# Kernel optimization log

Hardware: AMD Instinct MI355X
Metric: run time of the kernel (lower is better)

The kernel has to match this reference:

```python
import jax, jax.numpy as jnp
import numpy as np

SPLINE_ORDER = 3
BN_EPS = 1e-5


def make_grid(grid_size, lo=-1.0, hi=1.0):
    # torch KANLinear grid: uniform on [lo,hi] extended by spline_order knots each side
    h = (hi - lo) / grid_size
    return jnp.arange(-SPLINE_ORDER, grid_size + SPLINE_ORDER + 1, dtype=jnp.float32) * h + lo


def b_splines(x, grid, k=SPLINE_ORDER):
    # x: [...], grid: [G+2k+1] -> bases [..., G+k] (Cox-de Boor recursion)
    x = x[..., None]
    bases = ((x >= grid[:-1]) & (x < grid[1:])).astype(x.dtype)
    for j in range(1, k + 1):
        left = (x - grid[: -(j + 1)]) / (grid[j:-1] - grid[: -(j + 1)])
        right = (grid[j + 1:] - x) / (grid[j + 1:] - grid[1:-j])
        bases = left * bases[..., :-1] + right * bases[..., 1:]
    return bases


def extract_patches(x, d):
    # 3x3 dilated sliding windows, stride 1, padding == dilation -> same HxW
    B, C, H, W = x.shape
    xp = jnp.pad(x, ((0, 0), (0, 0), (d, d), (d, d)))
    pats = [xp[:, :, ki * d:ki * d + H, kj * d:kj * d + W]
            for ki in range(3) for kj in range(3)]
    return jnp.stack(pats, axis=-1)  # [B,C,H,W,9] (kh-major, matching torch Unfold)


def batchnorm(x, g, b):
    # training-mode BN (torch default forward): batch statistics, biased variance
    mean = x.mean(axis=(0, 2, 3), keepdims=True)
    var = x.var(axis=(0, 2, 3), keepdims=True)
    return (x - mean) / jnp.sqrt(var + BN_EPS) * g[None, :, None, None] + b[None, :, None, None]


def se_block(x, w1, w2):
    y = x.mean(axis=(2, 3))                                  # [B,C]
    y = jax.nn.sigmoid(jax.nn.relu(y @ w1.T) @ w2.T)         # [B,C]
    return x * y[:, :, None, None]


def kan_conv(x, base_w, spline_w, grid, dilation):
    # one KANLinear(9->1) per (out,in) channel pair, summed over in channels
    p = extract_patches(x, dilation)                          # [B,Ci,H,W,9]
    base = jnp.einsum('bihwk,oik->bohw', jax.nn.silu(p), base_w)
    bs = b_splines(p, grid)                                   # [B,Ci,H,W,9,G+k]
    spl = jnp.einsum('bihwkg,oikg->bohw', bs, spline_w)
    return base + spl


def kan_branch(x, base_w, spline_w, grid, dilation, bn_g, bn_b, se_w1, se_w2):
    y = kan_conv(x, base_w, spline_w, grid, dilation)
    y = jax.nn.relu(batchnorm(y, bn_g, bn_b))
    return se_block(y, se_w1, se_w2)


def setup_inputs() -> dict:
    key = jax.random.key(0)
    ks = jax.random.split(key, 16)
    B, Ci, Co, H, W = 2, 64, 64, 64, 64
    r = Co // 16
    d = {"x": jax.random.normal(ks[0], (B, Ci, H, W), jnp.float32)}
    for i, (bname, G) in enumerate([(6, 3), (12, 6), (18, 9)]):
        kk = jax.random.split(ks[1 + i], 4)
        d[f"base_w{bname}"] = jax.random.normal(kk[0], (Co, Ci, 9), jnp.float32) / np.sqrt(9.0 * Ci)
        d[f"spline_w{bname}"] = jax.random.normal(kk[1], (Co, Ci, 9, G + SPLINE_ORDER), jnp.float32) * (0.1 / np.sqrt(9.0 * Ci))
        d[f"bn{bname}_g"] = jnp.ones((Co,), jnp.float32)
        d[f"bn{bname}_b"] = jnp.zeros((Co,), jnp.float32)
        d[f"se{bname}_w1"] = jax.random.normal(kk[2], (r, Co), jnp.float32) / np.sqrt(Co)
        d[f"se{bname}_w2"] = jax.random.normal(kk[3], (Co, r), jnp.float32) / np.sqrt(r)
    d["gp_conv_w"] = jax.random.normal(ks[4], (Co, Ci), jnp.float32) / np.sqrt(Ci)
    d["gp_conv_b"] = jnp.zeros((Co,), jnp.float32)
    d["gp_bn_g"] = jnp.ones((Co,), jnp.float32)
    d["gp_bn_b"] = jnp.zeros((Co,), jnp.float32)
    d["gp_se_w1"] = jax.random.normal(ks[5], (r, Co), jnp.float32) / np.sqrt(Co)
    d["gp_se_w2"] = jax.random.normal(ks[6], (Co, r), jnp.float32) / np.sqrt(r)
    d["fuse_w"] = jax.random.normal(ks[7], (Co, 4 * Co), jnp.float32) / np.sqrt(4.0 * Co)
    d["fuse_b"] = jnp.zeros((Co,), jnp.float32)
    d["fuse_bn_g"] = jnp.ones((Co,), jnp.float32)
    d["fuse_bn_b"] = jnp.zeros((Co,), jnp.float32)
    return d


def reference(x, base_w6, spline_w6, bn6_g, bn6_b, se6_w1, se6_w2,
              base_w12, spline_w12, bn12_g, bn12_b, se12_w1, se12_w2,
              base_w18, spline_w18, bn18_g, bn18_b, se18_w1, se18_w2,
              gp_conv_w, gp_conv_b, gp_bn_g, gp_bn_b, gp_se_w1, gp_se_w2,
              fuse_w, fuse_b, fuse_bn_g, fuse_bn_b):
    B, Ci, H, W = x.shape
    # global-pool branch: avgpool -> 1x1 conv -> BN -> ReLU -> SE -> bilinear
    # upsample (1x1 source => pure broadcast, align_corners irrelevant)
    gp = x.mean(axis=(2, 3)) @ gp_conv_w.T + gp_conv_b      # [B,Co]
    gp = gp[:, :, None, None]
    gp = jax.nn.relu(batchnorm(gp, gp_bn_g, gp_bn_b))
    gp = se_block(gp, gp_se_w1, gp_se_w2)
    gp = jnp.broadcast_to(gp, (B, gp.shape[1], H, W))
    # KAN dilated branches
    b6 = kan_branch(x, base_w6, spline_w6, make_grid(3), 6, bn6_g, bn6_b, se6_w1, se6_w2)
    b12 = kan_branch(x, base_w12, spline_w12, make_grid(6), 12, bn12_g, bn12_b, se12_w1, se12_w2)
    b18 = kan_branch(x, base_w18, spline_w18, make_grid(9), 18, bn18_g, bn18_b, se18_w1, se18_w2)
    cat = jnp.concatenate([b6, b12, b18, gp], axis=1)        # [B,4Co,H,W]
    out = jnp.einsum('bihw,oi->bohw', cat, fuse_w) + fuse_b[None, :, None, None]
    out = jax.nn.relu(batchnorm(out, fuse_bn_g, fuse_bn_b))
    return out
```

## Files before the change

### kernel.cpp

```cpp
#include <hip/hip_runtime.h>
#include <hip/hip_bf16.h>
#include <math.h>

#define DEV __device__ __forceinline__

static constexpr int HW  = 4096;
static constexpr int POS = 8192;
static constexpr int SLAB = 6 * 64 * 4096;

typedef __attribute__((ext_vector_type(8)))  short short8;
typedef __attribute__((ext_vector_type(16))) float floatx16;
typedef __attribute__((ext_vector_type(4)))  unsigned int uint4v;

template<int G>
DEV void bsplines(float x, float* out ) {
  const float h = 2.0f / (float)G;
  float knot[G + 7];
#pragma unroll
  for (int t = 0; t < G + 7; ++t) knot[t] = -1.0f + (float)(t - 3) * h;
  float bb[G + 6];
#pragma unroll
  for (int t = 0; t < G + 6; ++t) bb[t] = (x >= knot[t] && x < knot[t + 1]) ? 1.0f : 0.0f;
#pragma unroll
  for (int j = 1; j <= 3; ++j) {
    const float inv = (float)G / (2.0f * (float)j);
#pragma unroll
    for (int t = 0; t < G + 6 - j; ++t) {
      float left  = (x - knot[t]) * inv;
      float right = (knot[t + j + 1] - x) * inv;
      bb[t] = left * bb[t] + right * bb[t + 1];
    }
  }
#pragma unroll
  for (int t = 0; t < G + 3; ++t) out[t] = bb[t];
}

DEV float sigmoidf_(float x) { return 1.0f / (1.0f + __expf(-x)); }

DEV float block_reduce_256(float v, float* sb) {
  __syncthreads();
#pragma unroll
  for (int off = 32; off > 0; off >>= 1) v += __shfl_down(v, off, 64);
  int lane = threadIdx.x & 63, wid = threadIdx.x >> 6;
  if (lane == 0) sb[wid] = v;
  __syncthreads();
  return sb[0] + sb[1] + sb[2] + sb[3];
}


template<int CF>
DEV void wprep_body(const float* __restrict__ base_w, const float* __restrict__ spline_w,
                    __hip_bfloat16* __restrict__ Wt, int bid) {
  constexpr int KC = 64 * CF;
  int lin = bid * 256 + threadIdx.x;
  int ic = lin % KC;
  int rest = lin / KC;
  int o = rest & 63, tap = rest >> 6;
  int c = ic % CF, i = ic / CF;
  float v = (c == 0) ? base_w[(o * 64 + i) * 9 + tap]
                     : spline_w[((o * 64 + i) * 9 + tap) * (CF - 1) + (c - 1)];
  int s = ic >> 4, kk = ic & 15, q = kk >> 3, r = kk & 7, hh = o >> 5;
  int l = q * 32 + (o & 31);
  Wt[(size_t)tap * (64 * KC) + s * 1024 + hh * 512 + l * 8 + r] = __float2bfloat16(v);
}

template<int G>
DEV void c0r_body(int ki, const float* __restrict__ sw, float* __restrict__ out,
                  float* shmem ) {
  constexpr int NB = G + 3;
  int o = threadIdx.x & 63, part = threadIdx.x >> 6;
  float b0[NB];
  bsplines<G>(0.0f, b0);
  float s = 0.0f;
  for (int kj = 0; kj < 3; ++kj) {
    int tap = ki * 3 + kj;
    for (int i = part * 16; i < part * 16 + 16; ++i) {
      const float* p = sw + ((size_t)(o * 64 + i) * 9 + tap) * NB;
#pragma unroll
      for (int c = 0; c < NB; ++c) s += p[c] * b0[c];
    }
  }
  shmem[part * 64 + o] = s;
  __syncthreads();
  if (part == 0)
    out[ki * 64 + o] = shmem[o] + shmem[64 + o] + shmem[128 + o] + shmem[192 + o];
}

template<int G, int RB>
DEV void feat_stage(float xv, float s, __hip_bfloat16* lds, int ws, int i) {
  constexpr int CF = G + 4;
  constexpr int RS = 64 * CF + 16;
  float bas[G + 3];
  bsplines<G>(xv, bas);
  __hip_bfloat16* d = lds + RB + ws * RS + i * CF;
  d[0] = __float2bfloat16(s);
#pragma unroll
  for (int c = 1; c < CF; ++c) d[c] = __float2bfloat16(bas[c - 1]);
}

template<int CF, int D, int RBu>
DEV void feat_copy(__hip_bfloat16* __restrict__ F, int b, int h, int wg, const uint4v* l) {
  constexpr int WP = 64 + 2 * D;
  constexpr int KC = 64 * CF;
  uint4v* g = (uint4v*)(F + (size_t)(b * 64 + h) * WP * KC);
  for (int t = threadIdx.x; t < 32 * CF; t += 256) {
    int sc = t >> 3, r = t & 7, wl = r >> 1, k4 = r & 1;
    g[(size_t)(sc * WP + D + wg * 4 + wl) * 2 + k4] = l[RBu + wl * (8 * CF + 2) + sc * 2 + k4];
  }
}

DEV void feat_interior(const float* __restrict__ x, __hip_bfloat16* F0, __hip_bfloat16* F1,
                       __hip_bfloat16* F2, int bid, __hip_bfloat16* lds) {
  int tid = threadIdx.x;
  int ws = tid & 3, i = tid >> 2;
  int wg = bid & 15, h = (bid >> 4) & 63, b = bid >> 10;
  int w = wg * 4 + ws;
  float xv = x[((size_t)(b * 64 + i) * 64 + h) * 64 + w];
  float s = xv * sigmoidf_(xv);
  feat_stage<3, 0>(xv, s, lds, ws, i);
  feat_stage<6, 1856>(xv, s, lds, ws, i);
  feat_stage<9, 4480>(xv, s, lds, ws, i);
  __syncthreads();
  const uint4v* l = (const uint4v*)lds;
  feat_copy<7, 6, 0>(F0, b, h, wg, l);
  feat_copy<10, 12, 232>(F1, b, h, wg, l);
  feat_copy<13, 18, 560>(F2, b, h, wg, l);
}

template<int G, int D>
DEV void halo_body(__hip_bfloat16* __restrict__ F, int bidl, __hip_bfloat16* ldsb) {
  constexpr int CF = G + 4;
  constexpr int WP = 64 + 2 * D;
  constexpr int KC = 64 * CF;
  constexpr int PW = 8 * CF;
  constexpr int D2 = 2 * D;
  int tid = threadIdx.x;
  float bas0[G + 3];
  bsplines<G>(0.0f, bas0);
  for (int k = tid; k < KC; k += 256) {
    int c = k % CF;
    float v = 0.0f;
#pragma unroll
    for (int cc = 1; cc < CF; ++cc) v = (c == cc) ? bas0[cc - 1] : v;
    ldsb[k] = __float2bfloat16(v);
  }
  __syncthreads();
  const uint4v* l = (const uint4v*)ldsb;
  uint4v* g = (uint4v*)F;
#pragma unroll
  for (int u = 0; u < 16; ++u) {
    int t = bidl * 4096 + u * 256 + tid;
    int rw = t / PW, r2 = t - rw * PW;
    int sc = r2 >> 1, k4 = r2 & 1;
    int row = rw / D2, wj = rw - row * D2;
    int wp = (wj < D) ? wj : 64 + wj;
    g[(size_t)row * (WP * KC / 8) + (size_t)(sc * WP + wp) * 2 + k4] = l[sc * 2 + k4];
  }
}

__global__ void prepfeat_k(const float* __restrict__ x,
                           __hip_bfloat16* F0, __hip_bfloat16* F1, __hip_bfloat16* F2,
                           const float* bw0, const float* sw0, const float* bw1,
                           const float* sw1, const float* bw2, const float* sw2,
                           __hip_bfloat16* W0, __hip_bfloat16* W1, __hip_bfloat16* W2,
                           float* C0r, const float* fuse_w, float* fwT,
                           float* xm, float* accz ) {
  __shared__ uint4v ldsq[984];
  __shared__ float shmem[256];
  __hip_bfloat16* lds = (__hip_bfloat16*)ldsq;
  int bid = blockIdx.x, tid = threadIdx.x;
  if (bid < 2048)      { feat_interior(x, F0, F1, F2, bid, lds); return; }
  else if (bid < 2069) { halo_body<3, 6>(F0, bid - 2048, lds); return; }
  else if (bid < 2129) { halo_body<6, 12>(F1, bid - 2069, lds); return; }
  else if (bid < 2246) { halo_body<9, 18>(F2, bid - 2129, lds); return; }
  int pb = bid - 2246;
  if (pb < 1008)      { wprep_body<7>(bw0, sw0, W0, pb); }
  else if (pb < 2448) { wprep_body<10>(bw1, sw1, W1, pb - 1008); }
  else if (pb < 4320) { wprep_body<13>(bw2, sw2, W2, pb - 2448); }
  else if (pb < 4329) {
    int idx = pb - 4320, br = idx / 3, ki = idx % 3;
    if (br == 0)      c0r_body<3>(ki, sw0, C0r, shmem);
    else if (br == 1) c0r_body<6>(ki, sw1, C0r + 192, shmem);
    else              c0r_body<9>(ki, sw2, C0r + 384, shmem);
  } else if (pb < 4377) {
    int lin = (pb - 4329) * 256 + tid;
    int o = lin & 63, i2 = lin >> 6;
    fwT[i2 * 64 + o] = fuse_w[o * 256 + i2];
  } else if (pb < 4505) {
    int bi = pb - 4377;
    const float* p = x + (size_t)bi * HW;
    float s = 0.0f;
    for (int t = tid; t < HW; t += 256) s += p[t];
    s = block_reduce_256(s, shmem);
    if (tid == 0) xm[bi] = s * (1.0f / HW);
  } else {
    for (int t = tid; t < 896; t += 256) accz[t] = 0.0f;
  }
}

DEV floatx16 mfma_bf16(short8 a, short8 b, floatx16 c) {
  return __builtin_amdgcn_mfma_f32_32x32x16_bf16(a, b, c, 0, 0, 0);
}

template<int CF, int DD>
DEV void conv_dev(int ki, int b, int hp, const short* __restrict__ F,
                  const short* __restrict__ W, const float* __restrict__ C0r,
                  float* __restrict__ ypart, int br, float* __restrict__ red) {
  constexpr int KC = 64 * CF;
  constexpr int WP = 64 + 2 * DD;
  int wid = threadIdx.x >> 6;
  int wv  = wid & 1;
  int kjw = wid >> 1;
  int lane = threadIdx.x & 63;
  int lr = lane & 31, lq = lane >> 5;
  int hs = hp * 2 + wv;
  int h_out = hs - (ki - 1) * DD;
  bool valid = (h_out >= 0 && h_out < 64);
  int h_tgt = valid ? h_out : (h_out < 0 ? h_out + 64 : h_out - 64);
  float* yb = ypart + (size_t)ki * SLAB + ((size_t)((br * 2 + b) * 64 + h_tgt)) * 4096;

  floatx16 acc[2][2];
#pragma unroll
  for (int ot = 0; ot < 2; ++ot)
#pragma unroll
    for (int wh = 0; wh < 2; ++wh)
#pragma unroll
      for (int r = 0; r < 16; ++r) acc[ot][wh][r] = 0.0f;

  if (valid) {
    const short* wl_ = W + (size_t)(ki * 3 + kjw) * (64 * KC) + lane * 8;
    const short* fB  = F + (size_t)(b * 64 + hs) * WP * KC
                         + (kjw * DD + lr) * 16 + lq * 8;
#pragma unroll 4
    for (int s = 0; s < 4 * CF; ++s) {
      short8 a0 = *(const short8*)(wl_ + s * 1024);
      short8 a1 = *(const short8*)(wl_ + s * 1024 + 512);
      short8 b0 = *(const short8*)(fB + s * (WP * 16));
      short8 b1 = *(const short8*)(fB + s * (WP * 16) + 512);
      acc[0][0] = mfma_bf16(a0, b0, acc[0][0]);
      acc[0][1] = mfma_bf16(a0, b1, acc[0][1]);
      acc[1][0] = mfma_bf16(a1, b0, acc[1][0]);
      acc[1][1] = mfma_bf16(a1, b1, acc[1][1]);
    }
  }

  float* slot = red + (size_t)wv * (64 * 65) + lane * 65;
  if (kjw == 2 && valid) {
#pragma unroll
    for (int ot = 0; ot < 2; ++ot)
#pragma unroll
      for (int wh = 0; wh < 2; ++wh)
#pragma unroll
        for (int r = 0; r < 16; ++r) slot[(ot * 2 + wh) * 16 + r] = acc[ot][wh][r];
  }
  __syncthreads();
  if (kjw == 1 && valid) {
#pragma unroll
    for (int ot = 0; ot < 2; ++ot)
#pragma unroll
      for (int wh = 0; wh < 2; ++wh)
#pragma unroll
        for (int r = 0; r < 16; ++r) {
          int idx = (ot * 2 + wh) * 16 + r;
          slot[idx] += acc[ot][wh][r];
        }
  }
  __syncthreads();
  if (kjw != 0) return;

  if (!valid) {
    const float* c0 = C0r + (br * 3 + ki) * 64;
#pragma unroll
    for (int wh = 0; wh < 2; ++wh) {
      int w = wh * 32 + lr;
#pragma unroll
      for (int ot = 0; ot < 2; ++ot)
#pragma unroll
        for (int r = 0; r < 16; ++r) {
          int o = (r & 3) + 8 * (r >> 2) + 4 * lq + 32 * ot;
          yb[(size_t)o * 64 + w] = c0[o];
        }
    }
    return;
  }

#pragma unroll
  for (int ot = 0; ot < 2; ++ot)
#pragma unroll
    for (int wh = 0; wh < 2; ++wh) {
      int w = wh * 32 + lr;
#pragma unroll
      for (int r = 0; r < 16; ++r) {
        int o = (r & 3) + 8 * (r >> 2) + 4 * lq + 32 * ot;
        yb[(size_t)o * 64 + w] = acc[ot][wh][r] + slot[(ot * 2 + wh) * 16 + r];
      }
    }
}

__global__ __launch_bounds__(384) void conv_all_k(
    const short* __restrict__ F0, const short* __restrict__ F1, const short* __restrict__ F2,
    const short* __restrict__ W0, const short* __restrict__ W1, const short* __restrict__ W2,
    const float* __restrict__ C0r, float* __restrict__ ypart) {
  __shared__ float red[2 * 64 * 65];
  int bid = blockIdx.x;
  int e  = bid & 7;
  int t  = bid >> 3;
  int ki = t % 3;
  int m  = (t / 3) * 8 + e;
  int br = m >> 6, b = (m >> 5) & 1, hp = m & 31;
  if (br == 0)      conv_dev<7, 6>(ki, b, hp, F0, W0, C0r, ypart, 0, red);
  else if (br == 1) conv_dev<10, 12>(ki, b, hp, F1, W1, C0r, ypart, 1, red);
  else              conv_dev<13, 18>(ki, b, hp, F2, W2, C0r, ypart, 2, red);
}

__global__ void rb_k(float* __restrict__ yp, float* __restrict__ bnacc_s,
                     float* __restrict__ bnacc_q) {
  int bid = blockIdx.x;
  int bb = bid / 256, chunk = bid % 256;
  int br = bb >> 1;
  int tid = threadIdx.x;
  size_t base = (size_t)bb * 262144 + chunk * 1024 + tid * 4;
  float4 v = *(const float4*)(yp + base);
#pragma unroll
  for (int s2 = 1; s2 < 3; ++s2) {
    float4 u = *(const float4*)(yp + base + (size_t)s2 * SLAB);
    v.x += u.x; v.y += u.y; v.z += u.z; v.w += u.w;
  }
  *(float4*)(yp + base) = v;
  float s = v.x + v.y + v.z + v.w;
  float q = v.x * v.x + v.y * v.y + v.z * v.z + v.w * v.w;
  s += __shfl_down(s, 8, 16); s += __shfl_down(s, 4, 16);
  s += __shfl_down(s, 2, 16); s += __shfl_down(s, 1, 16);
  q += __shfl_down(q, 8, 16); q += __shfl_down(q, 4, 16);
  q += __shfl_down(q, 2, 16); q += __shfl_down(q, 1, 16);
  if ((tid & 15) == 0) {
    int o = (chunk * 16 + (tid >> 4)) & 63;
    atomicAdd(&bnacc_s[br * 64 + o], s);
    atomicAdd(&bnacc_q[br * 64 + o], q);
  }
}

__global__ void sesum_k(const float* __restrict__ y, const float* __restrict__ bnacc_s,
                        const float* __restrict__ bnacc_q,
                        const float* g0, const float* b0p, const float* g1, const float* b1p,
                        const float* g2, const float* b2p, float* __restrict__ se_acc) {
  int bid = blockIdx.x;
  int bb = bid >> 6, h = bid & 63;
  int br = bb >> 1;
  int tid = threadIdx.x;
  int o = tid >> 2, wq = tid & 3;
  const float* gptr = (br == 0) ? g0 : ((br == 1) ? g1 : g2);
  const float* bptr = (br == 0) ? b0p : ((br == 1) ? b1p : b2p);
  float mu = bnacc_s[br * 64 + o] * (1.0f / POS);
  float var = bnacc_q[br * 64 + o] * (1.0f / POS) - mu * mu;
  float kk = gptr[o] / sqrtf(var + 1e-5f);
  float cc = bptr[o] - mu * kk;
  const float* row = y + (size_t)bb * 262144 + (size_t)h * 4096 + o * 64 + wq * 16;
  float s = 0.0f;
#pragma unroll
  for (int j = 0; j < 4; ++j) {
    float4 v = *(const float4*)(row + j * 4);
    float a;
    a = v.x * kk + cc; s += (a > 0.0f) ? a : 0.0f;
    a = v.y * kk + cc; s += (a > 0.0f) ? a : 0.0f;
    a = v.z * kk + cc; s += (a > 0.0f) ? a : 0.0f;
    a = v.w * kk + cc; s += (a > 0.0f) ? a : 0.0f;
  }
  s += __shfl_down(s, 2, 4);
  s += __shfl_down(s, 1, 4);
  if (wq == 0) atomicAdd(&se_acc[bb * 64 + o], s);
}

__global__ void semlp_gp_k(const float* __restrict__ se_acc,
                           const float* __restrict__ bnacc_s, const float* __restrict__ bnacc_q,
                           const float* g0, const float* b0p, const float* g1, const float* b1p,
                           const float* g2, const float* b2p,
                           const float* w10, const float* w11, const float* w12,
                           const float* w20, const float* w21, const float* w22,
                           float* __restrict__ A1, float* __restrict__ A0,
                           const float* __restrict__ xm, const float* __restrict__ gw,
                           const float* __restrict__ gb, const float* __restrict__ bng,
                           const float* __restrict__ bnb, const float* __restrict__ gpw1,
                           const float* __restrict__ gpw2, const float* __restrict__ fuse_w,
                           float* __restrict__ fuse_gp) {
  __shared__ float sm[64];
  __shared__ float g0s[2][64], gp1s[2][64], gpvs[2][64];
  int tid = threadIdx.x;
  if (blockIdx.x < 6) {
    int bb = blockIdx.x, br = bb >> 1;
    const float* w1 = (br == 0) ? w10 : ((br == 1) ? w11 : w12);
    const float* w2 = (br == 0) ? w20 : ((br == 1) ? w21 : w22);
    const float* gptr = (br == 0) ? g0 : ((br == 1) ? g1 : g2);
    const float* bptr = (br == 0) ? b0p : ((br == 1) ? b1p : b2p);
    if (tid < 64) sm[tid] = se_acc[bb * 64 + tid] * (1.0f / HW);
    __syncthreads();
    if (tid < 64) {
      int o = tid;
      float z[4];
#pragma unroll
      for (int j = 0; j < 4; ++j) {
        float s = 0.0f;
        for (int c2 = 0; c2 < 64; ++c2) s += sm[c2] * w1[j * 64 + c2];
        z[j] = (s > 0.0f) ? s : 0.0f;
      }
      float t = 0.0f;
#pragma unroll
      for (int j = 0; j < 4; ++j) t += z[j] * w2[o * 4 + j];
      t = sigmoidf_(t);
      float mu = bnacc_s[br * 64 + o] * (1.0f / POS);
      float var = bnacc_q[br * 64 + o] * (1.0f / POS) - mu * mu;
      float kk = gptr[o] / sqrtf(var + 1e-5f);
      float cc = bptr[o] - mu * kk;
      A1[bb * 64 + o] = kk * t;
      A0[bb * 64 + o] = cc * t;
    }
  } else {
    int b = tid >> 6, o = tid & 63;
    float gv = gb[o];
    for (int i = 0; i < 64; ++i) gv += xm[b * 64 + i] * gw[o * 64 + i];
    g0s[b][o] = gv;
    __syncthreads();
    float mu = 0.5f * (g0s[0][o] + g0s[1][o]);
    float df = g0s[0][o] - g0s[1][o];
    float var = 0.25f * df * df;
    float v = (gv - mu) / sqrtf(var + 1e-5f) * bng[o] + bnb[o];
    v = (v > 0.0f) ? v : 0.0f;
    gp1s[b][o] = v;
    __syncthreads();
    float z[4];
#pragma unroll
    for (int j = 0; j < 4; ++j) {
      float s = 0.0f;
      for (int c2 = 0; c2 < 64; ++c2) s += gp1s[b][c2] * gpw1[j * 64 + c2];
      z[j] = (s > 0.0f) ? s : 0.0f;
    }
    float t = 0.0f;
#pragma unroll
    for (int j = 0; j < 4; ++j) t += z[j] * gpw2[o * 4 + j];
    t = sigmoidf_(t);
    gpvs[b][o] = v * t;
    __syncthreads();
    float fg = 0.0f;
    for (int c2 = 0; c2 < 64; ++c2) fg += fuse_w[o * 256 + 192 + c2] * gpvs[b][c2];
    fuse_gp[b * 64 + o] = fg;
  }
}

__global__ __launch_bounds__(256) void fuse_k(
    const float* __restrict__ y, const float* __restrict__ A1, const float* __restrict__ A0,
    const float* __restrict__ fwT, const float* __restrict__ fb, const float* __restrict__ fgp,
    float* __restrict__ tmp, float* __restrict__ fstat) {
  int bid = blockIdx.x;
  int b = bid >> 7, h = (bid >> 1) & 63, wh = bid & 1;
  int tid = threadIdx.x;
  int wg = tid & 7, og = tid >> 3;
  int w0 = wg * 4, o0 = og * 2;
  float acc[2][4] = {};
  __shared__ float As[64][32];
  __shared__ float Ws[64][64];
  for (int br = 0; br < 3; ++br) {
#pragma unroll
    for (int m = 0; m < 8; ++m) {
      int lin = tid + m * 256;
      int oc = lin >> 5, wl = lin & 31;
      float v = y[(size_t)(br * 2 + b) * 262144 + (size_t)h * 4096 + oc * 64 + wh * 32 + wl];
      float a1 = A1[(br * 2 + b) * 64 + oc], a0 = A0[(br * 2 + b) * 64 + oc];
      v = v * a1 + a0;
      As[oc][wl] = (v > 0.0f) ? v : 0.0f;
    }
#pragma unroll
    for (int m = 0; m < 16; ++m) {
      int lin = tid + m * 256;
      int oc = lin >> 6, ol = lin & 63;
      Ws[oc][ol] = fwT[(br * 64 + oc) * 64 + ol];
    }
    __syncthreads();
#pragma unroll 8
    for (int ict = 0; ict < 64; ++ict) {
      float4 a = *reinterpret_cast<const float4*>(&As[ict][w0]);
      float2 wv = *reinterpret_cast<const float2*>(&Ws[ict][o0]);
      acc[0][0] += wv.x * a.x; acc[0][1] += wv.x * a.y; acc[0][2] += wv.x * a.z; acc[0][3] += wv.x * a.w;
      acc[1][0] += wv.y * a.x; acc[1][1] += wv.y * a.y; acc[1][2] += wv.y * a.z; acc[1][3] += wv.y * a.w;
    }
    __syncthreads();
  }
  float* tp = tmp + (size_t)(b * 64 + h) * 4096 + wh * 32;
  float ps[2], pq[2];
#pragma unroll
  for (int oo = 0; oo < 2; ++oo) {
    int o = o0 + oo;
    float bias = fb[o] + fgp[b * 64 + o];
    float4 v = make_float4(acc[oo][0] + bias, acc[oo][1] + bias,
                           acc[oo][2] + bias, acc[oo][3] + bias);
    *reinterpret_cast<float4*>(&tp[o * 64 + w0]) = v;
    ps[oo] = v.x + v.y + v.z + v.w;
    pq[oo] = v.x * v.x + v.y * v.y + v.z * v.z + v.w * v.w;
  }
  __syncthreads();
#pragma unroll
  for (int oo = 0; oo < 2; ++oo) { As[o0 + oo][wg] = ps[oo]; Ws[o0 + oo][wg] = pq[oo]; }
  __syncthreads();
  if (tid < 64) {
    float s = 0.0f, q = 0.0f;
#pragma unroll
    for (int r = 0; r < 8; ++r) { s += As[tid][r]; q += Ws[tid][r]; }
    atomicAdd(&fstat[tid], s);
    atomicAdd(&fstat[64 + tid], q);
  }
}

__global__ void final_k(const float* __restrict__ tmp, const float* __restrict__ fstat,
                        const float* __restrict__ g, const float* __restrict__ bb,
                        float* __restrict__ out) {
  int lin = blockIdx.x * 256 + threadIdx.x;
  int w = lin & 63, h2 = (lin >> 6) & 63, o = (lin >> 12) & 63, b = lin >> 18;
  float v = tmp[((size_t)(b * 64 + h2) * 64 + o) * 64 + w];
  float m = fstat[o] * (1.0f / POS);
  float var = fstat[64 + o] * (1.0f / POS) - m * m;
  float kk = g[o] / sqrtf(var + 1e-5f);
  float r = (v - m) * kk + bb[o];
  out[lin] = (r > 0.0f) ? r : 0.0f;
}

extern "C" void kernel_launch(void* const* d_in, const int* in_sizes, int n_in,
                              void* d_out, int out_size, void* d_ws, size_t ws_size,
                              hipStream_t stream) {
  const float* x = (const float*)d_in[0];
  const float* base_w[3]   = {(const float*)d_in[1],  (const float*)d_in[7],  (const float*)d_in[13]};
  const float* spline_w[3] = {(const float*)d_in[2],  (const float*)d_in[8],  (const float*)d_in[14]};
  const float* bn_g[3]     = {(const float*)d_in[3],  (const float*)d_in[9],  (const float*)d_in[15]};
  const float* bn_b[3]     = {(const float*)d_in[4],  (const float*)d_in[10], (const float*)d_in[16]};
  const float* se_w1[3]    = {(const float*)d_in[5],  (const float*)d_in[11], (const float*)d_in[17]};
  const float* se_w2[3]    = {(const float*)d_in[6],  (const float*)d_in[12], (const float*)d_in[18]};
  const float* gp_conv_w = (const float*)d_in[19];
  const float* gp_conv_b = (const float*)d_in[20];
  const float* gp_bn_g   = (const float*)d_in[21];
  const float* gp_bn_b   = (const float*)d_in[22];
  const float* gp_se_w1  = (const float*)d_in[23];
  const float* gp_se_w2  = (const float*)d_in[24];
  const float* fuse_w    = (const float*)d_in[25];
  const float* fuse_b    = (const float*)d_in[26];
  const float* fuse_bn_g = (const float*)d_in[27];
  const float* fuse_bn_b = (const float*)d_in[28];
  float* out = (float*)d_out;

  char* wsp = (char*)d_ws;
  auto alloc = [&](size_t bytes) -> char* {
    char* p = wsp;
    wsp += (bytes + 255) & ~(size_t)255;
    return p;
  };
  __hip_bfloat16* F0 = (__hip_bfloat16*)alloc((size_t)2 * 64 * 76 * 448 * 2);
  __hip_bfloat16* F1 = (__hip_bfloat16*)alloc((size_t)2 * 64 * 88 * 640 * 2);
  __hip_bfloat16* F2 = (__hip_bfloat16*)alloc((size_t)2 * 64 * 100 * 832 * 2);
  __hip_bfloat16* W0 = (__hip_bfloat16*)alloc((size_t)9 * 64 * 448 * 2);
  __hip_bfloat16* W1 = (__hip_bfloat16*)alloc((size_t)9 * 64 * 640 * 2);
  __hip_bfloat16* W2 = (__hip_bfloat16*)alloc((size_t)9 * 64 * 832 * 2);
  float* C0r   = (float*)alloc((size_t)3 * 3 * 64 * 4);
  float* ypart = (float*)alloc((size_t)3 * SLAB * 4);
  float* y     = ypart;
  float* tmp   = ypart + SLAB;
  float* A1  = (float*)alloc(384 * 4);
  float* A0  = (float*)alloc(384 * 4);
  float* xm  = (float*)alloc(128 * 4);
  float* fgp = (float*)alloc(128 * 4);
  float* fwT = (float*)alloc((size_t)12288 * 4);
  float* accz = (float*)alloc(896 * 4);
  float* fstat   = accz;
  float* bnacc_s = accz + 128;
  float* bnacc_q = accz + 320;
  float* se_acc  = accz + 512;

  prepfeat_k<<<6752, 256, 0, stream>>>(x, F0, F1, F2,
                                       base_w[0], spline_w[0], base_w[1], spline_w[1],
                                       base_w[2], spline_w[2], W0, W1, W2, C0r,
                                       fuse_w, fwT, xm, accz);
  conv_all_k<<<576, 384, 0, stream>>>(
      (const short*)F0, (const short*)F1, (const short*)F2,
      (const short*)W0, (const short*)W1, (const short*)W2, C0r, ypart);
  rb_k<<<1536, 256, 0, stream>>>(ypart, bnacc_s, bnacc_q);
  sesum_k<<<384, 256, 0, stream>>>(y, bnacc_s, bnacc_q, bn_g[0], bn_b[0], bn_g[1], bn_b[1],
                                   bn_g[2], bn_b[2], se_acc);
  semlp_gp_k<<<7, 128, 0, stream>>>(se_acc, bnacc_s, bnacc_q, bn_g[0], bn_b[0], bn_g[1], bn_b[1],
                                    bn_g[2], bn_b[2], se_w1[0], se_w1[1], se_w1[2],
                                    se_w2[0], se_w2[1], se_w2[2], A1, A0,
                                    xm, gp_conv_w, gp_conv_b, gp_bn_g, gp_bn_b,
                                    gp_se_w1, gp_se_w2, fuse_w, fgp);
  fuse_k<<<256, 256, 0, stream>>>(y, A1, A0, fwT, fuse_b, fgp, tmp, fstat);
  final_k<<<2048, 256, 0, stream>>>(tmp, fstat, fuse_bn_g, fuse_bn_b, out);
}
```

Measured before the change: 243.1 us.

## Fold SE MLP and global-pool branch into fuse kernel; vectorize weight prep

The small semlp_gp kernel is removed. Each fuse_k block now recomputes the SE gate coefficients, BN scale and shift, and the global-pool branch contribution in shared memory before its GEMM, which saves one launch and the global round trip for A1/A0/fgp. Separately, weight preparation now packs 8 bf16 values per thread into one 16-byte store, cutting the prep grid from 6752 to 2972 blocks. In exchange, each of the 256 fuse blocks repeats the tiny MLP work, adding serial latency at the start of every block.

```diff
diff --git a/kernel.cpp b/kernel.cpp
--- a/kernel.cpp
+++ b/kernel.cpp
@@ -52,16 +52,23 @@
 DEV void wprep_body(const float* __restrict__ base_w, const float* __restrict__ spline_w,
                     __hip_bfloat16* __restrict__ Wt, int bid) {
   constexpr int KC = 64 * CF;
-  int lin = bid * 256 + threadIdx.x;
+  int lin = (bid * 256 + threadIdx.x) * 8;
   int ic = lin % KC;
   int rest = lin / KC;
   int o = rest & 63, tap = rest >> 6;
-  int c = ic % CF, i = ic / CF;
-  float v = (c == 0) ? base_w[(o * 64 + i) * 9 + tap]
-                     : spline_w[((o * 64 + i) * 9 + tap) * (CF - 1) + (c - 1)];
-  int s = ic >> 4, kk = ic & 15, q = kk >> 3, r = kk & 7, hh = o >> 5;
+  short8 vout;
+#pragma unroll
+  for (int e = 0; e < 8; ++e) {
+    int ice = ic + e;
+    int c = ice % CF, i = ice / CF;
+    float v = (c == 0) ? base_w[(o * 64 + i) * 9 + tap]
+                       : spline_w[((o * 64 + i) * 9 + tap) * (CF - 1) + (c - 1)];
+    __hip_bfloat16 bv = __float2bfloat16(v);
+    vout[e] = *reinterpret_cast<short*>(&bv);
+  }
+  int s = ic >> 4, q = (ic & 15) >> 3, hh = o >> 5;
   int l = q * 32 + (o & 31);
-  Wt[(size_t)tap * (64 * KC) + s * 1024 + hh * 512 + l * 8 + r] = __float2bfloat16(v);
+  *(short8*)(Wt + (size_t)tap * (64 * KC) + s * 1024 + hh * 512 + l * 8) = vout;
 }
 
 template<int G>
@@ -174,20 +181,20 @@
   else if (bid < 2129) { halo_body<6, 12>(F1, bid - 2069, lds); return; }
   else if (bid < 2246) { halo_body<9, 18>(F2, bid - 2129, lds); return; }
   int pb = bid - 2246;
-  if (pb < 1008)      { wprep_body<7>(bw0, sw0, W0, pb); }
-  else if (pb < 2448) { wprep_body<10>(bw1, sw1, W1, pb - 1008); }
-  else if (pb < 4320) { wprep_body<13>(bw2, sw2, W2, pb - 2448); }
-  else if (pb < 4329) {
-    int idx = pb - 4320, br = idx / 3, ki = idx % 3;
+  if (pb < 126)       { wprep_body<7>(bw0, sw0, W0, pb); }
+  else if (pb < 306)  { wprep_body<10>(bw1, sw1, W1, pb - 126); }
+  else if (pb < 540)  { wprep_body<13>(bw2, sw2, W2, pb - 306); }
+  else if (pb < 549) {
+    int idx = pb - 540, br = idx / 3, ki = idx % 3;
     if (br == 0)      c0r_body<3>(ki, sw0, C0r, shmem);
     else if (br == 1) c0r_body<6>(ki, sw1, C0r + 192, shmem);
     else              c0r_body<9>(ki, sw2, C0r + 384, shmem);
-  } else if (pb < 4377) {
-    int lin = (pb - 4329) * 256 + tid;
+  } else if (pb < 597) {
+    int lin = (pb - 549) * 256 + tid;
     int o = lin & 63, i2 = lin >> 6;
     fwT[i2 * 64 + o] = fuse_w[o * 256 + i2];
-  } else if (pb < 4505) {
-    int bi = pb - 4377;
+  } else if (pb < 725) {
+    int bi = pb - 597;
     const float* p = x + (size_t)bi * HW;
     float s = 0.0f;
     for (int t = tid; t < HW; t += 256) s += p[t];
@@ -371,101 +378,103 @@
   if (wq == 0) atomicAdd(&se_acc[bb * 64 + o], s);
 }
 
-__global__ void semlp_gp_k(const float* __restrict__ se_acc,
-                           const float* __restrict__ bnacc_s, const float* __restrict__ bnacc_q,
-                           const float* g0, const float* b0p, const float* g1, const float* b1p,
-                           const float* g2, const float* b2p,
-                           const float* w10, const float* w11, const float* w12,
-                           const float* w20, const float* w21, const float* w22,
-                           float* __restrict__ A1, float* __restrict__ A0,
-                           const float* __restrict__ xm, const float* __restrict__ gw,
-                           const float* __restrict__ gb, const float* __restrict__ bng,
-                           const float* __restrict__ bnb, const float* __restrict__ gpw1,
-                           const float* __restrict__ gpw2, const float* __restrict__ fuse_w,
-                           float* __restrict__ fuse_gp) {
-  __shared__ float sm[64];
-  __shared__ float g0s[2][64], gp1s[2][64], gpvs[2][64];
-  int tid = threadIdx.x;
-  if (blockIdx.x < 6) {
-    int bb = blockIdx.x, br = bb >> 1;
-    const float* w1 = (br == 0) ? w10 : ((br == 1) ? w11 : w12);
-    const float* w2 = (br == 0) ? w20 : ((br == 1) ? w21 : w22);
-    const float* gptr = (br == 0) ? g0 : ((br == 1) ? g1 : g2);
-    const float* bptr = (br == 0) ? b0p : ((br == 1) ? b1p : b2p);
-    if (tid < 64) sm[tid] = se_acc[bb * 64 + tid] * (1.0f / HW);
-    __syncthreads();
-    if (tid < 64) {
-      int o = tid;
-      float z[4];
-#pragma unroll
-      for (int j = 0; j < 4; ++j) {
-        float s = 0.0f;
-        for (int c2 = 0; c2 < 64; ++c2) s += sm[c2] * w1[j * 64 + c2];
-        z[j] = (s > 0.0f) ? s : 0.0f;
-      }
-      float t = 0.0f;
-#pragma unroll
-      for (int j = 0; j < 4; ++j) t += z[j] * w2[o * 4 + j];
-      t = sigmoidf_(t);
-      float mu = bnacc_s[br * 64 + o] * (1.0f / POS);
-      float var = bnacc_q[br * 64 + o] * (1.0f / POS) - mu * mu;
-      float kk = gptr[o] / sqrtf(var + 1e-5f);
-      float cc = bptr[o] - mu * kk;
-      A1[bb * 64 + o] = kk * t;
-      A0[bb * 64 + o] = cc * t;
-    }
-  } else {
-    int b = tid >> 6, o = tid & 63;
-    float gv = gb[o];
-    for (int i = 0; i < 64; ++i) gv += xm[b * 64 + i] * gw[o * 64 + i];
-    g0s[b][o] = gv;
-    __syncthreads();
-    float mu = 0.5f * (g0s[0][o] + g0s[1][o]);
-    float df = g0s[0][o] - g0s[1][o];
-    float var = 0.25f * df * df;
-    float v = (gv - mu) / sqrtf(var + 1e-5f) * bng[o] + bnb[o];
-    v = (v > 0.0f) ? v : 0.0f;
-    gp1s[b][o] = v;
-    __syncthreads();
-    float z[4];
-#pragma unroll
-    for (int j = 0; j < 4; ++j) {
-      float s = 0.0f;
-      for (int c2 = 0; c2 < 64; ++c2) s += gp1s[b][c2] * gpw1[j * 64 + c2];
-      z[j] = (s > 0.0f) ? s : 0.0f;
-    }
-    float t = 0.0f;
-#pragma unroll
-    for (int j = 0; j < 4; ++j) t += z[j] * gpw2[o * 4 + j];
-    t = sigmoidf_(t);
-    gpvs[b][o] = v * t;
-    __syncthreads();
-    float fg = 0.0f;
-    for (int c2 = 0; c2 < 64; ++c2) fg += fuse_w[o * 256 + 192 + c2] * gpvs[b][c2];
-    fuse_gp[b * 64 + o] = fg;
-  }
-}
-
 __global__ __launch_bounds__(256) void fuse_k(
-    const float* __restrict__ y, const float* __restrict__ A1, const float* __restrict__ A0,
-    const float* __restrict__ fwT, const float* __restrict__ fb, const float* __restrict__ fgp,
+    const float* __restrict__ y, const float* __restrict__ fwT, const float* __restrict__ fb,
+    const float* __restrict__ se_acc, const float* __restrict__ bnacc_s,
+    const float* __restrict__ bnacc_q,
+    const float* g0, const float* b0p, const float* g1, const float* b1p,
+    const float* g2, const float* b2p,
+    const float* w10, const float* w11, const float* w12,
+    const float* w20, const float* w21, const float* w22,
+    const float* __restrict__ xm, const float* gw, const float* gb,
+    const float* bng, const float* bnb, const float* gpw1, const float* gpw2,
+    const float* __restrict__ fuse_w,
     float* __restrict__ tmp, float* __restrict__ fstat) {
   int bid = blockIdx.x;
   int b = bid >> 7, h = (bid >> 1) & 63, wh = bid & 1;
   int tid = threadIdx.x;
+  __shared__ float As[64][32];
+  __shared__ float Ws[64][64];
+  __shared__ float A1s[3][64], A0s[3][64], fgps[64];
+  __shared__ float pro[3][64], gp1v[64], gpv2[64];
+
+  int grp = tid >> 6, po = tid & 63;
+  float gv = 0.0f, gv_other = 0.0f;
+  if (grp < 3) {
+    pro[grp][po] = se_acc[(grp * 2 + b) * 64 + po] * (1.0f / HW);
+  } else {
+    float g_[2];
+#pragma unroll
+    for (int b2 = 0; b2 < 2; ++b2) {
+      float s = gb[po];
+      for (int i = 0; i < 64; ++i) s += xm[b2 * 64 + i] * gw[po * 64 + i];
+      g_[b2] = s;
+    }
+    gv = g_[b]; gv_other = g_[1 - b];
+  }
+  __syncthreads();
+  float v_gp = 0.0f;
+  if (grp < 3) {
+    const float* w1 = (grp == 0) ? w10 : ((grp == 1) ? w11 : w12);
+    const float* w2 = (grp == 0) ? w20 : ((grp == 1) ? w21 : w22);
+    const float* gptr = (grp == 0) ? g0 : ((grp == 1) ? g1 : g2);
+    const float* bptr = (grp == 0) ? b0p : ((grp == 1) ? b1p : b2p);
+    float z[4];
+#pragma unroll
+    for (int j = 0; j < 4; ++j) {
+      float s = 0.0f;
+      for (int c2 = 0; c2 < 64; ++c2) s += pro[grp][c2] * w1[j * 64 + c2];
+      z[j] = (s > 0.0f) ? s : 0.0f;
+    }
+    float t = 0.0f;
+#pragma unroll
+    for (int j = 0; j < 4; ++j) t += z[j] * w2[po * 4 + j];
+    t = sigmoidf_(t);
+    float mu = bnacc_s[grp * 64 + po] * (1.0f / POS);
+    float var = bnacc_q[grp * 64 + po] * (1.0f / POS) - mu * mu;
+    float kk = gptr[po] / sqrtf(var + 1e-5f);
+    float cc = bptr[po] - mu * kk;
+    A1s[grp][po] = kk * t;
+    A0s[grp][po] = cc * t;
+  } else {
+    float mu = 0.5f * (gv + gv_other);
+    float df = gv - gv_other;
+    float var = 0.25f * df * df;
+    v_gp = (gv - mu) / sqrtf(var + 1e-5f) * bng[po] + bnb[po];
+    v_gp = (v_gp > 0.0f) ? v_gp : 0.0f;
+    gp1v[po] = v_gp;
+  }
+  __syncthreads();
+  if (grp == 3) {
+    float z[4];
+#pragma unroll
+    for (int j = 0; j < 4; ++j) {
+      float s = 0.0f;
+      for (int c2 = 0; c2 < 64; ++c2) s += gp1v[c2] * gpw1[j * 64 + c2];
+      z[j] = (s > 0.0f) ? s : 0.0f;
+    }
+    float t = 0.0f;
+#pragma unroll
+    for (int j = 0; j < 4; ++j) t += z[j] * gpw2[po * 4 + j];
+    gpv2[po] = v_gp * sigmoidf_(t);
+  }
+  __syncthreads();
+  if (grp == 3) {
+    float fg = 0.0f;
+    for (int c2 = 0; c2 < 64; ++c2) fg += fuse_w[po * 256 + 192 + c2] * gpv2[c2];
+    fgps[po] = fg;
+  }
+
   int wg = tid & 7, og = tid >> 3;
   int w0 = wg * 4, o0 = og * 2;
   float acc[2][4] = {};
-  __shared__ float As[64][32];
-  __shared__ float Ws[64][64];
   for (int br = 0; br < 3; ++br) {
 #pragma unroll
     for (int m = 0; m < 8; ++m) {
       int lin = tid + m * 256;
       int oc = lin >> 5, wl = lin & 31;
       float v = y[(size_t)(br * 2 + b) * 262144 + (size_t)h * 4096 + oc * 64 + wh * 32 + wl];
-      float a1 = A1[(br * 2 + b) * 64 + oc], a0 = A0[(br * 2 + b) * 64 + oc];
-      v = v * a1 + a0;
+      v = v * A1s[br][oc] + A0s[br][oc];
       As[oc][wl] = (v > 0.0f) ? v : 0.0f;
     }
 #pragma unroll
@@ -489,7 +498,7 @@
 #pragma unroll
   for (int oo = 0; oo < 2; ++oo) {
     int o = o0 + oo;
-    float bias = fb[o] + fgp[b * 64 + o];
+    float bias = fb[o] + fgps[o];
     float4 v = make_float4(acc[oo][0] + bias, acc[oo][1] + bias,
                            acc[oo][2] + bias, acc[oo][3] + bias);
     *reinterpret_cast<float4*>(&tp[o * 64 + w0]) = v;
@@ -560,10 +569,7 @@
   float* ypart = (float*)alloc((size_t)3 * SLAB * 4);
   float* y     = ypart;
   float* tmp   = ypart + SLAB;
-  float* A1  = (float*)alloc(384 * 4);
-  float* A0  = (float*)alloc(384 * 4);
   float* xm  = (float*)alloc(128 * 4);
-  float* fgp = (float*)alloc(128 * 4);
   float* fwT = (float*)alloc((size_t)12288 * 4);
   float* accz = (float*)alloc(896 * 4);
   float* fstat   = accz;
@@ -571,7 +577,7 @@
   float* bnacc_q = accz + 320;
   float* se_acc  = accz + 512;
 
-  prepfeat_k<<<6752, 256, 0, stream>>>(x, F0, F1, F2,
+  prepfeat_k<<<2972, 256, 0, stream>>>(x, F0, F1, F2,
                                        base_w[0], spline_w[0], base_w[1], spline_w[1],
                                        base_w[2], spline_w[2], W0, W1, W2, C0r,
                                        fuse_w, fwT, xm, accz);
@@ -581,11 +587,10 @@
   rb_k<<<1536, 256, 0, stream>>>(ypart, bnacc_s, bnacc_q);
   sesum_k<<<384, 256, 0, stream>>>(y, bnacc_s, bnacc_q, bn_g[0], bn_b[0], bn_g[1], bn_b[1],
                                    bn_g[2], bn_b[2], se_acc);
-  semlp_gp_k<<<7, 128, 0, stream>>>(se_acc, bnacc_s, bnacc_q, bn_g[0], bn_b[0], bn_g[1], bn_b[1],
-                                    bn_g[2], bn_b[2], se_w1[0], se_w1[1], se_w1[2],
-                                    se_w2[0], se_w2[1], se_w2[2], A1, A0,
-                                    xm, gp_conv_w, gp_conv_b, gp_bn_g, gp_bn_b,
-                                    gp_se_w1, gp_se_w2, fuse_w, fgp);
-  fuse_k<<<256, 256, 0, stream>>>(y, A1, A0, fwT, fuse_b, fgp, tmp, fstat);
+  fuse_k<<<256, 256, 0, stream>>>(y, fwT, fuse_b, se_acc, bnacc_s, bnacc_q,
+                                  bn_g[0], bn_b[0], bn_g[1], bn_b[1], bn_g[2], bn_b[2],
+                                  se_w1[0], se_w1[1], se_w1[2], se_w2[0], se_w2[1], se_w2[2],
+                                  xm, gp_conv_w, gp_conv_b, gp_bn_g, gp_bn_b,
+                                  gp_se_w1, gp_se_w2, fuse_w, tmp, fstat);
   final_k<<<2048, 256, 0, stream>>>(tmp, fstat, fuse_bn_g, fuse_bn_b, out);
 }
```

New measurement: 246.9 us. Within noise of the previous version (+1.6%).
